# Kernel optimization log

Measured on AMD Instinct MI355X. Metric: run time of the kernel, lower is better.

The kernel has to match this reference:

```python
import jax, jax.numpy as jnp
import numpy as np

# Rows of A/B form separable 3x3 filters via outer product:
#   f0 = identity, f1 = sobel_y, f2 = sobel_x
_A = np.array([[0, 1, 0], [1, 0, -1], [1, 2, 1]], dtype=np.float32)
_B = np.array([[0, 1, 0], [1, 2, 1], [1, 0, -1]], dtype=np.float32)
_LAP = np.array([[0, -1, 0], [-1, 4, -1], [0, -1, 0]], dtype=np.float32)  # 4-connected Laplacian


def _fixed_kernels(C):
    # separable depthwise kernels, torch grouped-conv channel-major order: out idx = c*3 + f
    sep = np.einsum('fi,fj->fij', _A, _B)                       # (3, 3, 3)
    sep_k = np.tile(sep[None], (C, 1, 1, 1)).reshape(C * 3, 1, 3, 3)
    lap_k = np.tile(_LAP[None, None], (C, 1, 1, 1))             # (C, 1, 3, 3)
    return jnp.asarray(sep_k), jnp.asarray(lap_k)


def _conv(xp, k, groups=1):
    # cross-correlation, VALID on already-padded input (matches torch F.conv2d)
    return jax.lax.conv_general_dilated(
        xp, k, window_strides=(1, 1), padding='VALID',
        dimension_numbers=('NCHW', 'OIHW', 'NCHW'),
        feature_group_count=groups)


def setup_inputs() -> dict:
    key = jax.random.key(0)
    k1, k2, k3 = jax.random.split(key, 3)
    N, C, H, W, F = 8, 64, 256, 256, 128
    x = jax.random.normal(k1, (N, C, H, W), dtype=jnp.float32)
    fan_in = C * 9
    W_learned = jax.random.uniform(k2, (F, C, 3, 3), jnp.float32,
                                   -1.0 / np.sqrt(fan_in), 1.0 / np.sqrt(fan_in))
    b_learned = jax.random.uniform(k3, (F,), jnp.float32,
                                   -1.0 / np.sqrt(fan_in), 1.0 / np.sqrt(fan_in))
    return {"x": x, "W_learned": W_learned, "b_learned": b_learned}


def reference(x, W_learned, b_learned):
    C = x.shape[1]
    sep_k, lap_k = _fixed_kernels(C)
    # replicate (edge) pad by 1 on H and W
    xp = jnp.pad(x, ((0, 0), (0, 0), (1, 1), (1, 1)), mode='edge')
    sep = _conv(xp, sep_k, groups=C)                 # (N, 3C, H, W)
    lap = _conv(xp, lap_k, groups=C)                 # (N, C,  H, W)
    learned = _conv(xp, W_learned) + b_learned[None, :, None, None]  # (N, F, H, W)
    return jnp.concatenate([sep, lap, learned], axis=1)
```

## Files before the change

### kernel.cpp

```cpp
#include <hip/hip_runtime.h>

#define HH 256
#define WW 256
#define CC 64
#define FF 128
#define NN 8
#define OUTC 384
#define HW (HH * WW)

typedef __attribute__((ext_vector_type(8))) short bf16x8;
typedef __attribute__((ext_vector_type(4))) float f32x4;

__device__ __forceinline__ int clampi(int v, int lo, int hi) {
    return v < lo ? lo : (v > hi ? hi : v);
}

static __device__ __forceinline__ unsigned short f2bf(float x) {
    unsigned u = __builtin_bit_cast(unsigned, x);
    u += 0x7FFFu + ((u >> 16) & 1u);
    return (unsigned short)(u >> 16);
}
static __device__ __forceinline__ unsigned packbf(float a, float b) {
    return (unsigned)f2bf(a) | ((unsigned)f2bf(b) << 16);
}
static __device__ __forceinline__ float bf2f(unsigned short s) {
    return __builtin_bit_cast(float, (unsigned)s << 16);
}
static __device__ __forceinline__ void nts(float* p, float a, float b, float c, float d) {
    f32x4 v = {a, b, c, d};
    __builtin_nontemporal_store(v, reinterpret_cast<f32x4*>(p));
}

__global__ __launch_bounds__(256) void wT_kernel(const float* __restrict__ Wl,
                                                 unsigned short* __restrict__ wsW) {
    int e = blockIdx.x * 256 + threadIdx.x;
    if (e >= 9216) return;
    int t = e >> 10;
    int rem = e & 1023;
    int kg = rem >> 7;
    int f = rem & 127;
    unsigned u[4];
#pragma unroll
    for (int j2 = 0; j2 < 4; ++j2) {
        float a = Wl[(size_t)f * 576 + (size_t)(kg * 8 + 2 * j2) * 9 + t];
        float b = Wl[(size_t)f * 576 + (size_t)(kg * 8 + 2 * j2 + 1) * 9 + t];
        u[j2] = packbf(a, b);
    }
    *reinterpret_cast<uint4*>(wsW + (size_t)e * 8) = make_uint4(u[0], u[1], u[2], u[3]);
}

__global__ __launch_bounds__(256) void pack_kernel(const float* __restrict__ x,
                                                   unsigned short* __restrict__ xt) {
    int b = blockIdx.x;
    int y = b & 255;
    int cg = (b >> 8) & 7;
    int n = b >> 11;
    int w = threadIdx.x;
    const float* xp = x + ((size_t)(n * CC + cg * 8)) * HW + (size_t)y * WW + w;
    unsigned u[4];
#pragma unroll
    for (int j2 = 0; j2 < 4; ++j2)
        u[j2] = packbf(xp[(size_t)(2 * j2) * HW], xp[(size_t)(2 * j2 + 1) * HW]);
    *reinterpret_cast<uint4*>(xt + ((size_t)((n * 8 + cg) * HH + y) * WW + w) * 8) =
        make_uint4(u[0], u[1], u[2], u[3]);
}

__global__ __launch_bounds__(256, 4) void learned_kernel(const unsigned short* __restrict__ wsW,
                                                         const unsigned short* __restrict__ xt,
                                                         const float* __restrict__ bl,
                                                         float* __restrict__ out) {
    __shared__ float lds_e[4][16][68];

    int bid = blockIdx.x;
    int q = ((bid & 7) << 9) | (bid >> 3);
    int xs = q & 1;
    int y = (q >> 1) & 255;
    int n = q >> 9;

    int tid = threadIdx.x;
    int lane = tid & 63;
    int w = tid >> 6;
    int wf = w >> 1;
    int ws = w & 1;
    int x0 = xs * 128 + ws * 64;
    int lr = lane & 15;
    int lk = lane >> 4;

    const char* xb = reinterpret_cast<const char*>(xt) + (size_t)n * (8 * HH * WW * 16);

    int colb[4][3];
#pragma unroll
    for (int j = 0; j < 4; ++j)
#pragma unroll
        for (int dx = 0; dx < 3; ++dx)
            colb[j][dx] = clampi(x0 + j * 16 + lr + dx - 1, 0, WW - 1) * 16;

    f32x4 acc[4][4] = {};

#pragma unroll
    for (int t = 0; t < 9; ++t) {
        int dy = t / 3, dx = t - 3 * (t / 3);
        int yc = clampi(y + dy - 1, 0, HH - 1);
#pragma unroll
        for (int kk = 0; kk < 2; ++kk) {
            int kg = kk * 4 + lk;
            size_t rowoff = ((size_t)kg * HH + yc) * (WW * 16);
            bf16x8 a4[4], b4[4];
#pragma unroll
            for (int mt = 0; mt < 4; ++mt)
                a4[mt] = *reinterpret_cast<const bf16x8*>(
                    wsW + ((size_t)(t * 8 + kg) * 128 + wf * 64 + mt * 16 + lr) * 8);
#pragma unroll
            for (int j = 0; j < 4; ++j)
                b4[j] = *reinterpret_cast<const bf16x8*>(xb + rowoff + colb[j][dx]);
#pragma unroll
            for (int mt = 0; mt < 4; ++mt)
#pragma unroll
                for (int j = 0; j < 4; ++j)
                    acc[mt][j] = __builtin_amdgcn_mfma_f32_16x16x32_bf16(
                        a4[mt], b4[j], acc[mt][j], 0, 0, 0);
        }
    }

    float* le = &lds_e[w][0][0];
#pragma unroll
    for (int mt = 0; mt < 4; ++mt) {
#pragma unroll
        for (int i = 0; i < 4; ++i) {
            int f16 = lk * 4 + i;
            float bv = bl[wf * 64 + mt * 16 + f16];
#pragma unroll
            for (int j = 0; j < 4; ++j)
                le[f16 * 68 + j * 16 + lr] = acc[mt][j][i] + bv;
        }
#pragma unroll
        for (int p = 0; p < 4; ++p) {
            int f16 = p * 4 + lk;
            const float* s = &le[f16 * 68 + lr * 4];
            int f = wf * 64 + mt * 16 + f16;
            nts(out + (size_t)(n * OUTC + 256 + f) * HW + (size_t)y * WW + x0 + lr * 4,
                s[0], s[1], s[2], s[3]);
        }
    }
}

__global__ __launch_bounds__(256) void dw_kernel(const unsigned short* __restrict__ xt,
                                                 float* __restrict__ out) {
    int bid = blockIdx.x;
    int b = ((bid & 7) << 11) | (bid >> 3);
    int y = b & 255;
    int cg = (b >> 8) & 7;
    int n = b >> 11;
    int w = threadIdx.x;

    const unsigned short* xg = xt + (size_t)(n * 8 + cg) * HH * WW * 8;
    int yr[3], wc[3];
#pragma unroll
    for (int d = 0; d < 3; ++d) {
        yr[d] = clampi(y + d - 1, 0, HH - 1);
        wc[d] = clampi(w + d - 1, 0, WW - 1);
    }
    uint4 chunk[3][3];
#pragma unroll
    for (int r = 0; r < 3; ++r)
#pragma unroll
        for (int c = 0; c < 3; ++c)
            chunk[r][c] = *reinterpret_cast<const uint4*>(
                xg + ((size_t)yr[r] * WW + wc[c]) * 8);

    size_t ob = (size_t)n * OUTC * HW + (size_t)y * WW + w;
#pragma unroll
    for (int j = 0; j < 8; ++j) {
        float v[3][3];
#pragma unroll
        for (int r = 0; r < 3; ++r)
#pragma unroll
            for (int c = 0; c < 3; ++c) {
                unsigned word = (&chunk[r][c].x)[j >> 1];
                v[r][c] = bf2f((unsigned short)(j & 1 ? word >> 16 : word & 0xffff));
            }
        int ch = cg * 8 + j;
        float tL = v[0][0], tC = v[0][1], tR = v[0][2];
        float mL = v[1][0], mC = v[1][1], mR = v[1][2];
        float bL = v[2][0], bC = v[2][1], bR = v[2][2];
        float o0 = mC;
        float o1 = (tL + 2.f * tC + tR) - (bL + 2.f * bC + bR);
        float o2 = (tL - tR) + 2.f * (mL - mR) + (bL - bR);
        float o3 = 4.f * mC - tC - bC - mL - mR;
        __builtin_nontemporal_store(o0, out + ob + (size_t)(ch * 3 + 0) * HW);
        __builtin_nontemporal_store(o1, out + ob + (size_t)(ch * 3 + 1) * HW);
        __builtin_nontemporal_store(o2, out + ob + (size_t)(ch * 3 + 2) * HW);
        __builtin_nontemporal_store(o3, out + ob + (size_t)(192 + ch) * HW);
    }
}

extern "C" void kernel_launch(void* const* d_in, const int* in_sizes, int n_in,
                              void* d_out, int out_size, void* d_ws, size_t ws_size,
                              hipStream_t stream) {
    const float* x  = (const float*)d_in[0];
    const float* Wl = (const float*)d_in[1];
    const float* bl = (const float*)d_in[2];
    float* out = (float*)d_out;

    unsigned short* wsW = (unsigned short*)d_ws;
    unsigned short* xt  = (unsigned short*)((char*)d_ws + 262144);

    wT_kernel<<<36, 256, 0, stream>>>(Wl, wsW);
    pack_kernel<<<16384, 256, 0, stream>>>(x, xt);
    learned_kernel<<<NN * 512, 256, 0, stream>>>(wsW, xt, bl, out);
    dw_kernel<<<16384, 256, 0, stream>>>(xt, out);
}
```

Before: 278.8 us.

## Fuse depthwise sobel/laplacian stencil into learned conv MFMA kernel

Removes the separate depthwise kernel and computes the fixed sobel, identity and Laplacian outputs inside the learned-conv kernel, interleaved with the MFMA tap loop. Each wave handles 4 of the 8 channels in each channel group for its 64 pixels, so one group is done per tap iteration. This saves a launch and an extra pass over the packed input, and lets the stencil stores overlap with MFMA compute. In exchange it adds register pressure and store traffic inside a kernel limited to 4 waves per SIMD, and does 8-byte gathers instead of 16-byte ones.

```diff
diff --git a/kernel.cpp b/kernel.cpp
--- a/kernel.cpp
+++ b/kernel.cpp
@@ -65,10 +65,10 @@
         make_uint4(u[0], u[1], u[2], u[3]);
 }
 
-__global__ __launch_bounds__(256, 4) void learned_kernel(const unsigned short* __restrict__ wsW,
-                                                         const unsigned short* __restrict__ xt,
-                                                         const float* __restrict__ bl,
-                                                         float* __restrict__ out) {
+__global__ __launch_bounds__(256, 4) void fused_kernel(const unsigned short* __restrict__ wsW,
+                                                       const unsigned short* __restrict__ xt,
+                                                       const float* __restrict__ bl,
+                                                       float* __restrict__ out) {
     __shared__ float lds_e[4][16][68];
 
     int bid = blockIdx.x;
@@ -95,6 +95,14 @@
         for (int dx = 0; dx < 3; ++dx)
             colb[j][dx] = clampi(x0 + j * 16 + lr + dx - 1, 0, WW - 1) * 16;
 
+    int pxg = x0 + lane;
+    int dwyr[3], dwwc[3];
+#pragma unroll
+    for (int d = 0; d < 3; ++d) {
+        dwyr[d] = clampi(y + d - 1, 0, HH - 1);
+        dwwc[d] = clampi(pxg + d - 1, 0, WW - 1);
+    }
+
     f32x4 acc[4][4] = {};
 
 #pragma unroll
@@ -119,6 +127,39 @@
                 for (int j = 0; j < 4; ++j)
                     acc[mt][j] = __builtin_amdgcn_mfma_f32_16x16x32_bf16(
                         a4[mt], b4[j], acc[mt][j], 0, 0, 0);
+        }
+
+        if (t < 8) {
+            int cg = t;
+            const char* cgbase = xb + (size_t)cg * HH * (WW * 16) + wf * 8;
+            uint2 c9[3][3];
+#pragma unroll
+            for (int r = 0; r < 3; ++r)
+#pragma unroll
+                for (int d = 0; d < 3; ++d)
+                    c9[r][d] = *reinterpret_cast<const uint2*>(
+                        cgbase + ((size_t)dwyr[r] * WW + dwwc[d]) * 16);
+            size_t ob = (size_t)n * OUTC * HW + (size_t)y * WW + pxg;
+#pragma unroll
+            for (int i = 0; i < 4; ++i) {
+                float v[3][3];
+#pragma unroll
+                for (int r = 0; r < 3; ++r)
+#pragma unroll
+                    for (int d = 0; d < 3; ++d) {
+                        unsigned word = (i < 2) ? c9[r][d].x : c9[r][d].y;
+                        v[r][d] = bf2f((unsigned short)((i & 1) ? (word >> 16) : (word & 0xffff)));
+                    }
+                int ch = cg * 8 + wf * 4 + i;
+                float o0 = v[1][1];
+                float o1 = (v[0][0] + 2.f * v[0][1] + v[0][2]) - (v[2][0] + 2.f * v[2][1] + v[2][2]);
+                float o2 = (v[0][0] - v[0][2]) + 2.f * (v[1][0] - v[1][2]) + (v[2][0] - v[2][2]);
+                float o3 = 4.f * v[1][1] - v[0][1] - v[2][1] - v[1][0] - v[1][2];
+                __builtin_nontemporal_store(o0, out + ob + (size_t)(ch * 3 + 0) * HW);
+                __builtin_nontemporal_store(o1, out + ob + (size_t)(ch * 3 + 1) * HW);
+                __builtin_nontemporal_store(o2, out + ob + (size_t)(ch * 3 + 2) * HW);
+                __builtin_nontemporal_store(o3, out + ob + (size_t)(192 + ch) * HW);
+            }
         }
     }
 
@@ -141,56 +182,6 @@
             nts(out + (size_t)(n * OUTC + 256 + f) * HW + (size_t)y * WW + x0 + lr * 4,
                 s[0], s[1], s[2], s[3]);
         }
-    }
-}
-
-__global__ __launch_bounds__(256) void dw_kernel(const unsigned short* __restrict__ xt,
-                                                 float* __restrict__ out) {
-    int bid = blockIdx.x;
-    int b = ((bid & 7) << 11) | (bid >> 3);
-    int y = b & 255;
-    int cg = (b >> 8) & 7;
-    int n = b >> 11;
-    int w = threadIdx.x;
-
-    const unsigned short* xg = xt + (size_t)(n * 8 + cg) * HH * WW * 8;
-    int yr[3], wc[3];
-#pragma unroll
-    for (int d = 0; d < 3; ++d) {
-        yr[d] = clampi(y + d - 1, 0, HH - 1);
-        wc[d] = clampi(w + d - 1, 0, WW - 1);
-    }
-    uint4 chunk[3][3];
-#pragma unroll
-    for (int r = 0; r < 3; ++r)
-#pragma unroll
-        for (int c = 0; c < 3; ++c)
-            chunk[r][c] = *reinterpret_cast<const uint4*>(
-                xg + ((size_t)yr[r] * WW + wc[c]) * 8);
-
-    size_t ob = (size_t)n * OUTC * HW + (size_t)y * WW + w;
-#pragma unroll
-    for (int j = 0; j < 8; ++j) {
-        float v[3][3];
-#pragma unroll
-        for (int r = 0; r < 3; ++r)
-#pragma unroll
-            for (int c = 0; c < 3; ++c) {
-                unsigned word = (&chunk[r][c].x)[j >> 1];
-                v[r][c] = bf2f((unsigned short)(j & 1 ? word >> 16 : word & 0xffff));
-            }
-        int ch = cg * 8 + j;
-        float tL = v[0][0], tC = v[0][1], tR = v[0][2];
-        float mL = v[1][0], mC = v[1][1], mR = v[1][2];
-        float bL = v[2][0], bC = v[2][1], bR = v[2][2];
-        float o0 = mC;
-        float o1 = (tL + 2.f * tC + tR) - (bL + 2.f * bC + bR);
-        float o2 = (tL - tR) + 2.f * (mL - mR) + (bL - bR);
-        float o3 = 4.f * mC - tC - bC - mL - mR;
-        __builtin_nontemporal_store(o0, out + ob + (size_t)(ch * 3 + 0) * HW);
-        __builtin_nontemporal_store(o1, out + ob + (size_t)(ch * 3 + 1) * HW);
-        __builtin_nontemporal_store(o2, out + ob + (size_t)(ch * 3 + 2) * HW);
-        __builtin_nontemporal_store(o3, out + ob + (size_t)(192 + ch) * HW);
     }
 }
 
@@ -207,6 +198,5 @@
 
     wT_kernel<<<36, 256, 0, stream>>>(Wl, wsW);
     pack_kernel<<<16384, 256, 0, stream>>>(x, xt);
-    learned_kernel<<<NN * 512, 256, 0, stream>>>(wsW, xt, bl, out);
-    dw_kernel<<<16384, 256, 0, stream>>>(xt, out);
-}
+    fused_kernel<<<NN * 512, 256, 0, stream>>>(wsW, xt, bl, out);
+}
```

Measured after the change: 255.9 us. 8.2% less time.
